# Kernel optimization log

Hardware: AMD Instinct MI355X
Metric: run time of the kernel (lower is better)

## Reference

```python
import jax, jax.numpy as jnp
import numpy as np

N_NODES = 50000
N_EDGES = 1600000
IN_CH = 128
HID = 128
LAT = 32


def _sage_conv(h, src, dst, W_l, W_r, b, num_nodes):
    # PyG SAGEConv: mean-aggregate neighbor (source) features at dst,
    # then lin_l(aggr) + lin_r(x) + bias
    msg = h[src]                                             # [E, d] irregular gather
    agg = jax.ops.segment_sum(msg, dst, num_segments=num_nodes)
    cnt = jax.ops.segment_sum(jnp.ones((src.shape[0], 1), h.dtype), dst,
                              num_segments=num_nodes)
    mean = agg / jnp.maximum(cnt, 1.0)
    return mean @ W_l + h @ W_r + b


def setup_inputs() -> dict:
    key = jax.random.key(0)
    ks = jax.random.split(key, 16)
    s = 0.05
    inp = {
        "x": jax.random.normal(ks[0], (N_NODES, IN_CH), jnp.float32),
        "edge_index": jax.random.randint(ks[1], (2, N_EDGES), 0, N_NODES, jnp.int32),
        "eps": jax.random.normal(ks[2], (N_NODES, LAT), jnp.float32),
        # SAGEConv layer 0
        "Wl0": jax.random.normal(ks[3], (IN_CH, HID), jnp.float32) * s,
        "Wr0": jax.random.normal(ks[4], (IN_CH, HID), jnp.float32) * s,
        "b0": jnp.zeros((HID,), jnp.float32),
        # SAGEConv layer 1
        "Wl1": jax.random.normal(ks[5], (HID, HID), jnp.float32) * s,
        "Wr1": jax.random.normal(ks[6], (HID, HID), jnp.float32) * s,
        "b1": jnp.zeros((HID,), jnp.float32),
        # mu / logvar heads
        "Wmu": jax.random.normal(ks[7], (HID, LAT), jnp.float32) * s,
        "bmu": jnp.zeros((LAT,), jnp.float32),
        "Wlv": jax.random.normal(ks[8], (HID, LAT), jnp.float32) * s,
        "blv": jnp.zeros((LAT,), jnp.float32),
    }
    return inp


def reference(x, edge_index, eps, Wl0, Wr0, b0, Wl1, Wr1, b1, Wmu, bmu, Wlv, blv):
    src, dst = edge_index[0], edge_index[1]
    n = x.shape[0]
    h = jax.nn.relu(_sage_conv(x, src, dst, Wl0, Wr0, b0, n))
    h = jax.nn.relu(_sage_conv(h, src, dst, Wl1, Wr1, b1, n))
    mu = h @ Wmu + bmu
    logvar = h @ Wlv + blv
    z = mu + eps * jnp.exp(0.5 * logvar)          # reparameterize
    probs = jax.nn.sigmoid(jnp.sum(z[src] * z[dst], axis=-1))  # edge decode
    return probs, mu, logvar
```

## Files before the change

kernel.cpp:

```cpp
#include <hip/hip_runtime.h>
#include <math.h>

#define NN 50000
#define NE 1600000
#define CH 128
#define LAT 32
#define NB 196

__device__ __forceinline__ unsigned short f2bf(float f) {
  unsigned int u = __float_as_uint(f);
  unsigned int r = u + 0x7FFFu + ((u >> 16) & 1u);
  return (unsigned short)(r >> 16);
}
__device__ __forceinline__ float bf2f(unsigned short s) {
  return __uint_as_float(((unsigned int)s) << 16);
}
__device__ __forceinline__ float bflo(unsigned int u) {
  return __uint_as_float(u << 16);
}
__device__ __forceinline__ float bfhi(unsigned int u) {
  return __uint_as_float(u & 0xffff0000u);
}

__global__ void k_tobf16(const float* __restrict__ in, unsigned short* __restrict__ out,
                         int n4) {
  int i = blockIdx.x * 256 + threadIdx.x;
  if (i < n4) {
    float4 v = reinterpret_cast<const float4*>(in)[i];
    ushort4 o;
    o.x = f2bf(v.x); o.y = f2bf(v.y); o.z = f2bf(v.z); o.w = f2bf(v.w);
    reinterpret_cast<ushort4*>(out)[i] = o;
  }
}

__global__ void k_hist(const int* __restrict__ dst, int* __restrict__ deg) {
  int e = blockIdx.x * 256 + threadIdx.x;
  if (e < NE) atomicAdd(&deg[dst[e]], 1);
}

__global__ void k_scan1(const int* __restrict__ deg, int* __restrict__ bsum) {
  __shared__ int red[256];
  int i = blockIdx.x * 256 + threadIdx.x;
  red[threadIdx.x] = (i < NN) ? deg[i] : 0;
  __syncthreads();
  for (int s = 128; s > 0; s >>= 1) {
    if (threadIdx.x < s) red[threadIdx.x] += red[threadIdx.x + s];
    __syncthreads();
  }
  if (threadIdx.x == 0) bsum[blockIdx.x] = red[0];
}

__global__ void k_scan2(const int* __restrict__ bsum, int* __restrict__ boff) {
  __shared__ int tmp[256];
  int t = threadIdx.x;
  int v = (t < NB) ? bsum[t] : 0;
  tmp[t] = v;
  __syncthreads();
  for (int off = 1; off < 256; off <<= 1) {
    int add = (t >= off) ? tmp[t - off] : 0;
    __syncthreads();
    tmp[t] += add;
    __syncthreads();
  }
  if (t < NB) boff[t] = tmp[t] - v;
}

__global__ void k_scan3(const int* __restrict__ deg, const int* __restrict__ boff,
                        int* __restrict__ row_start, int* __restrict__ cursor) {
  __shared__ int tmp[256];
  int t = threadIdx.x;
  int i = blockIdx.x * 256 + t;
  int v = (i < NN) ? deg[i] : 0;
  tmp[t] = v;
  __syncthreads();
  for (int off = 1; off < 256; off <<= 1) {
    int add = (t >= off) ? tmp[t - off] : 0;
    __syncthreads();
    tmp[t] += add;
    __syncthreads();
  }
  int excl = tmp[t] - v + boff[blockIdx.x];
  if (i < NN) { row_start[i] = excl; cursor[i] = excl; }
}

__global__ void k_fill(const int* __restrict__ src, const int* __restrict__ dst,
                       int* __restrict__ cursor, int* __restrict__ eid) {
  int e = blockIdx.x * 256 + threadIdx.x;
  if (e < NE) {
    int d = dst[e];
    int pos = atomicAdd(&cursor[d], 1);
    eid[pos] = src[e];
  }
}

__global__ __launch_bounds__(256, 8) void k_sage2(
    const unsigned short* __restrict__ featb, const float* __restrict__ feat32,
    const int* __restrict__ deg, const int* __restrict__ row_start,
    const int* __restrict__ eid,
    const float* __restrict__ Wl, const float* __restrict__ Wr,
    const float* __restrict__ bias, unsigned short* __restrict__ outb) {
  __shared__ __align__(16) unsigned short mean_t[128][36];
  __shared__ __align__(16) unsigned short h_t[128][36];
  int tid = threadIdx.x;
  int nbase = blockIdx.x * 32;
  int hw = tid >> 5, q = tid & 31;
  int q4 = q * 4;

  for (int n = hw; n < 32; n += 8) {
    int v = nbase + n;
    float ax = 0.f, ay = 0.f, az = 0.f, aw = 0.f;
    float hx = 0.f, hy = 0.f, hz = 0.f, hwv = 0.f;
    if (v < NN) {
      int r0 = row_start[v];
      int dg = deg[v];
      int i = 0;
      for (; i + 3 < dg; i += 4) {
        int s0 = eid[r0 + i + 0];
        int s1 = eid[r0 + i + 1];
        int s2 = eid[r0 + i + 2];
        int s3 = eid[r0 + i + 3];
        ushort4 a = *reinterpret_cast<const ushort4*>(featb + (size_t)s0 * CH + q4);
        ushort4 b = *reinterpret_cast<const ushort4*>(featb + (size_t)s1 * CH + q4);
        ushort4 c = *reinterpret_cast<const ushort4*>(featb + (size_t)s2 * CH + q4);
        ushort4 d = *reinterpret_cast<const ushort4*>(featb + (size_t)s3 * CH + q4);
        ax += bf2f(a.x) + bf2f(b.x) + bf2f(c.x) + bf2f(d.x);
        ay += bf2f(a.y) + bf2f(b.y) + bf2f(c.y) + bf2f(d.y);
        az += bf2f(a.z) + bf2f(b.z) + bf2f(c.z) + bf2f(d.z);
        aw += bf2f(a.w) + bf2f(b.w) + bf2f(c.w) + bf2f(d.w);
      }
      for (; i < dg; ++i) {
        int s0 = eid[r0 + i];
        ushort4 a = *reinterpret_cast<const ushort4*>(featb + (size_t)s0 * CH + q4);
        ax += bf2f(a.x); ay += bf2f(a.y); az += bf2f(a.z); aw += bf2f(a.w);
      }
      float r = 1.0f / (float)max(dg, 1);
      ax *= r; ay *= r; az *= r; aw *= r;
      if (feat32) {
        float4 hh = *reinterpret_cast<const float4*>(feat32 + (size_t)v * CH + q4);
        hx = hh.x; hy = hh.y; hz = hh.z; hwv = hh.w;
      } else {
        ushort4 hb = *reinterpret_cast<const ushort4*>(featb + (size_t)v * CH + q4);
        hx = bf2f(hb.x); hy = bf2f(hb.y); hz = bf2f(hb.z); hwv = bf2f(hb.w);
      }
    }
    mean_t[q4 + 0][n] = f2bf(ax);
    mean_t[q4 + 1][n] = f2bf(ay);
    mean_t[q4 + 2][n] = f2bf(az);
    mean_t[q4 + 3][n] = f2bf(aw);
    h_t[q4 + 0][n] = f2bf(hx);
    h_t[q4 + 1][n] = f2bf(hy);
    h_t[q4 + 2][n] = f2bf(hz);
    h_t[q4 + 3][n] = f2bf(hwv);
  }
  __syncthreads();

  int jg = tid & 31, ng = tid >> 5;
  int j0 = jg * 4, nl = ng * 4;
  float acc[4][4];
#pragma unroll
  for (int a = 0; a < 4; a++)
#pragma unroll
    for (int b = 0; b < 4; b++) acc[a][b] = 0.f;

#pragma unroll 2
  for (int k = 0; k < 128; ++k) {
    float4 wl = *reinterpret_cast<const float4*>(Wl + k * CH + j0);
    float4 wr = *reinterpret_cast<const float4*>(Wr + k * CH + j0);
    uint2 mp = *reinterpret_cast<const uint2*>(&mean_t[k][nl]);
    uint2 hp = *reinterpret_cast<const uint2*>(&h_t[k][nl]);
    float mn[4] = {bflo(mp.x), bfhi(mp.x), bflo(mp.y), bfhi(mp.y)};
    float hn[4] = {bflo(hp.x), bfhi(hp.x), bflo(hp.y), bfhi(hp.y)};
#pragma unroll
    for (int n = 0; n < 4; ++n) {
      acc[n][0] += mn[n] * wl.x + hn[n] * wr.x;
      acc[n][1] += mn[n] * wl.y + hn[n] * wr.y;
      acc[n][2] += mn[n] * wl.z + hn[n] * wr.z;
      acc[n][3] += mn[n] * wl.w + hn[n] * wr.w;
    }
  }

  float4 bb = *reinterpret_cast<const float4*>(bias + j0);
#pragma unroll
  for (int n = 0; n < 4; ++n) {
    int v = nbase + nl + n;
    if (v < NN) {
      ushort4 ob;
      ob.x = f2bf(fmaxf(acc[n][0] + bb.x, 0.f));
      ob.y = f2bf(fmaxf(acc[n][1] + bb.y, 0.f));
      ob.z = f2bf(fmaxf(acc[n][2] + bb.z, 0.f));
      ob.w = f2bf(fmaxf(acc[n][3] + bb.w, 0.f));
      *reinterpret_cast<ushort4*>(outb + (size_t)v * CH + j0) = ob;
    }
  }
}

__global__ __launch_bounds__(256) void k_heads(
    const unsigned short* __restrict__ h2b, const float* __restrict__ eps,
    const float* __restrict__ Wmu, const float* __restrict__ bmu,
    const float* __restrict__ Wlv, const float* __restrict__ blv,
    float* __restrict__ mu_out, float* __restrict__ lv_out,
    unsigned short* __restrict__ zb) {
  __shared__ float hs[32][132];
  int tid = threadIdx.x;
  int nbase = blockIdx.x * 32;

  for (int f = tid; f < 1024; f += 256) {
    int row = f >> 5;
    int c4 = (f & 31) * 4;
    int v = nbase + row;
    float4 hh = make_float4(0.f, 0.f, 0.f, 0.f);
    if (v < NN) {
      ushort4 hb = *reinterpret_cast<const ushort4*>(h2b + (size_t)v * CH + c4);
      hh = make_float4(bf2f(hb.x), bf2f(hb.y), bf2f(hb.z), bf2f(hb.w));
    }
    *reinterpret_cast<float4*>(&hs[row][c4]) = hh;
  }
  __syncthreads();

  int n = tid >> 3;
  int j0 = (tid & 7) * 4;
  float am[4] = {0.f, 0.f, 0.f, 0.f};
  float al[4] = {0.f, 0.f, 0.f, 0.f};
#pragma unroll 4
  for (int k = 0; k < 128; ++k) {
    float4 wm = *reinterpret_cast<const float4*>(Wmu + k * LAT + j0);
    float4 wv = *reinterpret_cast<const float4*>(Wlv + k * LAT + j0);
    float hv = hs[n][k];
    am[0] += hv * wm.x; am[1] += hv * wm.y; am[2] += hv * wm.z; am[3] += hv * wm.w;
    al[0] += hv * wv.x; al[1] += hv * wv.y; al[2] += hv * wv.z; al[3] += hv * wv.w;
  }
  int v = nbase + n;
  if (v < NN) {
    float4 bm = *reinterpret_cast<const float4*>(bmu + j0);
    float4 bl = *reinterpret_cast<const float4*>(blv + j0);
    float4 e4 = *reinterpret_cast<const float4*>(eps + (size_t)v * LAT + j0);
    float4 mu, lv;
    mu.x = am[0] + bm.x; mu.y = am[1] + bm.y; mu.z = am[2] + bm.z; mu.w = am[3] + bm.w;
    lv.x = al[0] + bl.x; lv.y = al[1] + bl.y; lv.z = al[2] + bl.z; lv.w = al[3] + bl.w;
    ushort4 zz;
    zz.x = f2bf(mu.x + e4.x * expf(0.5f * lv.x));
    zz.y = f2bf(mu.y + e4.y * expf(0.5f * lv.y));
    zz.z = f2bf(mu.z + e4.z * expf(0.5f * lv.z));
    zz.w = f2bf(mu.w + e4.w * expf(0.5f * lv.w));
    *reinterpret_cast<float4*>(mu_out + (size_t)v * LAT + j0) = mu;
    *reinterpret_cast<float4*>(lv_out + (size_t)v * LAT + j0) = lv;
    *reinterpret_cast<ushort4*>(zb + (size_t)v * LAT + j0) = zz;
  }
}

__global__ void k_decode(const int* __restrict__ src, const int* __restrict__ dst,
                         const unsigned short* __restrict__ zb,
                         float* __restrict__ probs) {
  int t = blockIdx.x * 256 + threadIdx.x;
  int e = t >> 3, part = t & 7;
  if (e >= NE) return;
  int s = src[e], d = dst[e];
  ushort4 a = *reinterpret_cast<const ushort4*>(zb + (size_t)s * LAT + part * 4);
  ushort4 b = *reinterpret_cast<const ushort4*>(zb + (size_t)d * LAT + part * 4);
  float p = bf2f(a.x) * bf2f(b.x) + bf2f(a.y) * bf2f(b.y) +
            bf2f(a.z) * bf2f(b.z) + bf2f(a.w) * bf2f(b.w);
  p += __shfl_xor(p, 1);
  p += __shfl_xor(p, 2);
  p += __shfl_xor(p, 4);
  if (part == 0) probs[e] = 1.0f / (1.0f + expf(-p));
}

extern "C" void kernel_launch(void* const* d_in, const int* in_sizes, int n_in,
                              void* d_out, int out_size, void* d_ws, size_t ws_size,
                              hipStream_t stream) {
  const float* x   = (const float*)d_in[0];
  const int*   ei  = (const int*)d_in[1];
  const float* eps = (const float*)d_in[2];
  const float* Wl0 = (const float*)d_in[3];
  const float* Wr0 = (const float*)d_in[4];
  const float* b0  = (const float*)d_in[5];
  const float* Wl1 = (const float*)d_in[6];
  const float* Wr1 = (const float*)d_in[7];
  const float* b1  = (const float*)d_in[8];
  const float* Wmu = (const float*)d_in[9];
  const float* bmu = (const float*)d_in[10];
  const float* Wlv = (const float*)d_in[11];
  const float* blv = (const float*)d_in[12];
  const int* src = ei;
  const int* dst = ei + NE;

  int* iws = (int*)d_ws;
  int* deg       = iws;
  int* row_start = deg + NN;
  int* cursor    = row_start + NN;
  int* bsum      = cursor + NN;
  int* boff      = bsum + 256;
  int* eid       = boff + 256;
  unsigned short* xb  = (unsigned short*)(eid + NE);
  unsigned short* h1b = xb + (size_t)NN * CH;
  unsigned short* h2b = h1b + (size_t)NN * CH;
  unsigned short* zb  = xb;

  float* probs  = (float*)d_out;
  float* mu_out = probs + NE;
  float* lv_out = mu_out + NN * LAT;

  hipMemsetAsync(deg, 0, NN * sizeof(int), stream);

  k_tobf16<<<(NN * CH / 4 + 255) / 256, 256, 0, stream>>>(x, xb, NN * CH / 4);
  k_hist <<<(NE + 255) / 256, 256, 0, stream>>>(dst, deg);
  k_scan1<<<NB, 256, 0, stream>>>(deg, bsum);
  k_scan2<<<1, 256, 0, stream>>>(bsum, boff);
  k_scan3<<<NB, 256, 0, stream>>>(deg, boff, row_start, cursor);
  k_fill <<<(NE + 255) / 256, 256, 0, stream>>>(src, dst, cursor, eid);

  k_sage2<<<(NN + 31) / 32, 256, 0, stream>>>(xb, x, deg, row_start, eid,
                                              Wl0, Wr0, b0, h1b);
  k_sage2<<<(NN + 31) / 32, 256, 0, stream>>>(h1b, nullptr, deg, row_start, eid,
                                              Wl1, Wr1, b1, h2b);

  k_heads<<<(NN + 31) / 32, 256, 0, stream>>>(h2b, eps, Wmu, bmu, Wlv, blv,
                                              mu_out, lv_out, zb);
  k_decode<<<(NE * 8 + 255) / 256, 256, 0, stream>>>(src, dst, zb, probs);
}
```

Measured before the change: 659.5 us.

## Shrink SAGE node tiles to 16, keep fp32 smem, deepen gather unroll, widen decode loads

The SAGE kernel now processes 16 nodes per block instead of 32. It keeps the aggregated mean and self features in fp32 shared memory in node-major layout rather than transposed bf16, and each thread computes 2 nodes by 4 outputs. The neighbor gather loop is unrolled by 8 with the indices loaded up front, to get more loads in flight. The decode kernel uses 4 threads per edge with 16-byte loads and one fewer shuffle stage. The intent is better gather latency hiding and more blocks, at the cost of reloading the weights from cache twice as often per node.

```diff
diff --git a/kernel.cpp b/kernel.cpp
--- a/kernel.cpp
+++ b/kernel.cpp
@@ -99,14 +99,14 @@
     const int* __restrict__ eid,
     const float* __restrict__ Wl, const float* __restrict__ Wr,
     const float* __restrict__ bias, unsigned short* __restrict__ outb) {
-  __shared__ __align__(16) unsigned short mean_t[128][36];
-  __shared__ __align__(16) unsigned short h_t[128][36];
+  __shared__ float mean_s[16][128];
+  __shared__ float h_s[16][128];
   int tid = threadIdx.x;
-  int nbase = blockIdx.x * 32;
+  int nbase = blockIdx.x * 16;
   int hw = tid >> 5, q = tid & 31;
   int q4 = q * 4;
 
-  for (int n = hw; n < 32; n += 8) {
+  for (int n = hw; n < 16; n += 8) {
     int v = nbase + n;
     float ax = 0.f, ay = 0.f, az = 0.f, aw = 0.f;
     float hx = 0.f, hy = 0.f, hz = 0.f, hwv = 0.f;
@@ -114,19 +114,15 @@
       int r0 = row_start[v];
       int dg = deg[v];
       int i = 0;
-      for (; i + 3 < dg; i += 4) {
-        int s0 = eid[r0 + i + 0];
-        int s1 = eid[r0 + i + 1];
-        int s2 = eid[r0 + i + 2];
-        int s3 = eid[r0 + i + 3];
-        ushort4 a = *reinterpret_cast<const ushort4*>(featb + (size_t)s0 * CH + q4);
-        ushort4 b = *reinterpret_cast<const ushort4*>(featb + (size_t)s1 * CH + q4);
-        ushort4 c = *reinterpret_cast<const ushort4*>(featb + (size_t)s2 * CH + q4);
-        ushort4 d = *reinterpret_cast<const ushort4*>(featb + (size_t)s3 * CH + q4);
-        ax += bf2f(a.x) + bf2f(b.x) + bf2f(c.x) + bf2f(d.x);
-        ay += bf2f(a.y) + bf2f(b.y) + bf2f(c.y) + bf2f(d.y);
-        az += bf2f(a.z) + bf2f(b.z) + bf2f(c.z) + bf2f(d.z);
-        aw += bf2f(a.w) + bf2f(b.w) + bf2f(c.w) + bf2f(d.w);
+      for (; i + 7 < dg; i += 8) {
+        int s[8];
+#pragma unroll
+        for (int u = 0; u < 8; ++u) s[u] = eid[r0 + i + u];
+#pragma unroll
+        for (int u = 0; u < 8; ++u) {
+          ushort4 a = *reinterpret_cast<const ushort4*>(featb + (size_t)s[u] * CH + q4);
+          ax += bf2f(a.x); ay += bf2f(a.y); az += bf2f(a.z); aw += bf2f(a.w);
+        }
       }
       for (; i < dg; ++i) {
         int s0 = eid[r0 + i];
@@ -143,45 +139,37 @@
         hx = bf2f(hb.x); hy = bf2f(hb.y); hz = bf2f(hb.z); hwv = bf2f(hb.w);
       }
     }
-    mean_t[q4 + 0][n] = f2bf(ax);
-    mean_t[q4 + 1][n] = f2bf(ay);
-    mean_t[q4 + 2][n] = f2bf(az);
-    mean_t[q4 + 3][n] = f2bf(aw);
-    h_t[q4 + 0][n] = f2bf(hx);
-    h_t[q4 + 1][n] = f2bf(hy);
-    h_t[q4 + 2][n] = f2bf(hz);
-    h_t[q4 + 3][n] = f2bf(hwv);
+    *reinterpret_cast<float4*>(&mean_s[n][q4]) = make_float4(ax, ay, az, aw);
+    *reinterpret_cast<float4*>(&h_s[n][q4]) = make_float4(hx, hy, hz, hwv);
   }
   __syncthreads();
 
   int jg = tid & 31, ng = tid >> 5;
-  int j0 = jg * 4, nl = ng * 4;
-  float acc[4][4];
-#pragma unroll
-  for (int a = 0; a < 4; a++)
+  int j0 = jg * 4, nl = ng * 2;
+  float acc[2][4];
+#pragma unroll
+  for (int a = 0; a < 2; a++)
 #pragma unroll
     for (int b = 0; b < 4; b++) acc[a][b] = 0.f;
 
-#pragma unroll 2
+#pragma unroll 4
   for (int k = 0; k < 128; ++k) {
     float4 wl = *reinterpret_cast<const float4*>(Wl + k * CH + j0);
     float4 wr = *reinterpret_cast<const float4*>(Wr + k * CH + j0);
-    uint2 mp = *reinterpret_cast<const uint2*>(&mean_t[k][nl]);
-    uint2 hp = *reinterpret_cast<const uint2*>(&h_t[k][nl]);
-    float mn[4] = {bflo(mp.x), bfhi(mp.x), bflo(mp.y), bfhi(mp.y)};
-    float hn[4] = {bflo(hp.x), bfhi(hp.x), bflo(hp.y), bfhi(hp.y)};
-#pragma unroll
-    for (int n = 0; n < 4; ++n) {
-      acc[n][0] += mn[n] * wl.x + hn[n] * wr.x;
-      acc[n][1] += mn[n] * wl.y + hn[n] * wr.y;
-      acc[n][2] += mn[n] * wl.z + hn[n] * wr.z;
-      acc[n][3] += mn[n] * wl.w + hn[n] * wr.w;
+#pragma unroll
+    for (int n = 0; n < 2; ++n) {
+      float m = mean_s[nl + n][k];
+      float hv = h_s[nl + n][k];
+      acc[n][0] += m * wl.x + hv * wr.x;
+      acc[n][1] += m * wl.y + hv * wr.y;
+      acc[n][2] += m * wl.z + hv * wr.z;
+      acc[n][3] += m * wl.w + hv * wr.w;
     }
   }
 
   float4 bb = *reinterpret_cast<const float4*>(bias + j0);
 #pragma unroll
-  for (int n = 0; n < 4; ++n) {
+  for (int n = 0; n < 2; ++n) {
     int v = nbase + nl + n;
     if (v < NN) {
       ushort4 ob;
@@ -252,16 +240,17 @@
                          const unsigned short* __restrict__ zb,
                          float* __restrict__ probs) {
   int t = blockIdx.x * 256 + threadIdx.x;
-  int e = t >> 3, part = t & 7;
+  int e = t >> 2, part = t & 3;
   if (e >= NE) return;
   int s = src[e], d = dst[e];
-  ushort4 a = *reinterpret_cast<const ushort4*>(zb + (size_t)s * LAT + part * 4);
-  ushort4 b = *reinterpret_cast<const ushort4*>(zb + (size_t)d * LAT + part * 4);
-  float p = bf2f(a.x) * bf2f(b.x) + bf2f(a.y) * bf2f(b.y) +
-            bf2f(a.z) * bf2f(b.z) + bf2f(a.w) * bf2f(b.w);
+  uint4 ua = *reinterpret_cast<const uint4*>(zb + (size_t)s * LAT + part * 8);
+  uint4 ub = *reinterpret_cast<const uint4*>(zb + (size_t)d * LAT + part * 8);
+  float p = bflo(ua.x) * bflo(ub.x) + bfhi(ua.x) * bfhi(ub.x)
+          + bflo(ua.y) * bflo(ub.y) + bfhi(ua.y) * bfhi(ub.y)
+          + bflo(ua.z) * bflo(ub.z) + bfhi(ua.z) * bfhi(ub.z)
+          + bflo(ua.w) * bflo(ub.w) + bfhi(ua.w) * bfhi(ub.w);
   p += __shfl_xor(p, 1);
   p += __shfl_xor(p, 2);
-  p += __shfl_xor(p, 4);
   if (part == 0) probs[e] = 1.0f / (1.0f + expf(-p));
 }
 
@@ -309,12 +298,12 @@
   k_scan3<<<NB, 256, 0, stream>>>(deg, boff, row_start, cursor);
   k_fill <<<(NE + 255) / 256, 256, 0, stream>>>(src, dst, cursor, eid);
 
-  k_sage2<<<(NN + 31) / 32, 256, 0, stream>>>(xb, x, deg, row_start, eid,
+  k_sage2<<<(NN + 15) / 16, 256, 0, stream>>>(xb, x, deg, row_start, eid,
                                               Wl0, Wr0, b0, h1b);
-  k_sage2<<<(NN + 31) / 32, 256, 0, stream>>>(h1b, nullptr, deg, row_start, eid,
+  k_sage2<<<(NN + 15) / 16, 256, 0, stream>>>(h1b, nullptr, deg, row_start, eid,
                                               Wl1, Wr1, b1, h2b);
 
   k_heads<<<(NN + 31) / 32, 256, 0, stream>>>(h2b, eps, Wmu, bmu, Wlv, blv,
                                               mu_out, lv_out, zb);
-  k_decode<<<(NE * 8 + 255) / 256, 256, 0, stream>>>(src, dst, zb, probs);
-}
+  k_decode<<<(NE * 4 + 255) / 256, 256, 0, stream>>>(src, dst, zb, probs);
+}
```

Result: no change. 669.6 us (+1.5%).
